# Optimization experiments

Hardware: AMD Instinct MI355X
Metric: run time of the kernel (lower is better)

## Reference

```python
import jax, jax.numpy as jnp
import numpy as np

B, S, D = 2, 2048, 1024          # batch, seq, hidden_dim
H, HD = 16, 64                   # heads, head_dim
R = 256                          # kv_lora_rank (MLA latent)
E, K, MH = 8, 2, 256             # n_experts, top_k, expert hidden
EPS = 1e-6
THETA = 10000.0


def setup_inputs() -> dict:
    key = jax.random.key(0)
    ks = jax.random.split(key, 11)
    init = lambda k, shape: jax.random.normal(k, shape, jnp.float32) * 0.02
    return {
        "x": jax.random.normal(ks[0], (B, S, D), jnp.float32),
        "position_ids": jnp.broadcast_to(jnp.arange(S, dtype=jnp.int32), (B, S)),
        "norm1_w": jnp.ones((D,), jnp.float32),
        "wq": init(ks[1], (D, H * HD)),
        "wdkv": init(ks[2], (D, R)),
        "wuk": init(ks[3], (R, H * HD)),
        "wuv": init(ks[4], (R, H * HD)),
        "wo": init(ks[5], (H * HD, D)),
        "norm2_w": jnp.ones((D,), jnp.float32),
        "wr": init(ks[6], (D, E)),
        "router_bias": jnp.zeros((E,), jnp.float32),
        "w1": init(ks[7], (E, D, MH)),
        "w3": init(ks[8], (E, D, MH)),
        "w2": init(ks[9], (E, MH, D)),
    }


def rmsnorm(x, w):
    var = jnp.mean(x * x, axis=-1, keepdims=True)
    return x * jax.lax.rsqrt(var + EPS) * w


def rope(q, k, pos):
    # q, k: [B,S,H,HD]; pos: [B,S]
    half = HD // 2
    inv = 1.0 / (THETA ** (jnp.arange(half, dtype=jnp.float32) / half))
    ang = pos[..., None].astype(jnp.float32) * inv        # [B,S,half]
    cos = jnp.cos(ang)[:, :, None, :]                     # [B,S,1,half]
    sin = jnp.sin(ang)[:, :, None, :]
    def rot(t):
        t1, t2 = t[..., :half], t[..., half:]
        return jnp.concatenate([t1 * cos - t2 * sin, t1 * sin + t2 * cos], -1)
    return rot(q), rot(k)


def mla_attention(x, pos, wq, wdkv, wuk, wuv, wo):
    q = (x @ wq).reshape(B, S, H, HD)
    c = x @ wdkv                                          # [B,S,R] latent KV
    k = (c @ wuk).reshape(B, S, H, HD)
    v = (c @ wuv).reshape(B, S, H, HD)
    q, k = rope(q, k, pos)
    scores = jnp.einsum('bqhd,bkhd->bhqk', q, k) / np.float32(np.sqrt(HD))
    causal = jnp.tril(jnp.ones((S, S), bool))
    scores = jnp.where(causal, scores, jnp.float32(-1e30))
    probs = jax.nn.softmax(scores, axis=-1)
    out = jnp.einsum('bhqk,bkhd->bqhd', probs, v).reshape(B, S, H * HD)
    return out @ wo


def self_adaptive_moe(x, wr, router_bias, w1, w3, w2):
    xf = x.reshape(-1, D)                                 # [T,D]
    scores = jax.nn.sigmoid(xf @ wr)                      # [T,E]
    # aux-loss-free balancing: bias only affects selection, not gate weights
    _, idx = jax.lax.top_k(scores + router_bias, K)       # [T,K]
    sel = jnp.take_along_axis(scores, idx, axis=1)        # [T,K]
    sel = sel / (jnp.sum(sel, -1, keepdims=True) + 1e-9)
    rows = jnp.arange(xf.shape[0])[:, None]
    gates = jnp.zeros_like(scores).at[rows, idx].set(sel)  # [T,E]
    y = jnp.zeros_like(xf)
    for e in range(E):  # small fixed expert count
        h = jax.nn.silu(xf @ w1[e]) * (xf @ w3[e])        # SwiGLU
        y = y + gates[:, e:e + 1] * (h @ w2[e])
    return y.reshape(B, S, D)


def reference(x, position_ids, norm1_w, wq, wdkv, wuk, wuv, wo,
              norm2_w, wr, router_bias, w1, w3, w2):
    x = x + mla_attention(rmsnorm(x, norm1_w), position_ids, wq, wdkv, wuk, wuv, wo)
    x = x + self_adaptive_moe(rmsnorm(x, norm2_w), wr, router_bias, w1, w3, w2)
    return x
```

## Files before the change

### kernel.cpp

```cpp
#include <hip/hip_runtime.h>
#include <hip/hip_bf16.h>
#include <math.h>


typedef __attribute__((ext_vector_type(8))) short short8;
typedef __attribute__((ext_vector_type(4))) float f32x4;

static __device__ __forceinline__ float bf2f(short s) {
  union { unsigned u; float f; } c; c.u = ((unsigned)(unsigned short)s) << 16; return c.f;
}
static __device__ __forceinline__ short f2bf(float f) {
  __hip_bfloat16 h = __float2bfloat16(f);
  short s; __builtin_memcpy(&s, &h, sizeof(s)); return s;
}
static __device__ __forceinline__ void split2(float v, short& hi, short& lo) {
  hi = f2bf(v); lo = f2bf(v - bf2f(hi));
}

__global__ void invtab_kernel(float* __restrict__ tab) {
  int j = threadIdx.x;
  if (j < 32) {
    float t = (float)pow(10000.0, (double)j * (1.0 / 32.0));
    tab[j] = 1.0f / t;
  }
}

__global__ __launch_bounds__(256) void rmsnorm_kernel(
    const float* __restrict__ in, const float* __restrict__ w,
    short* __restrict__ outH, short* __restrict__ outL,
    float* __restrict__ invrms)
{
  int row = blockIdx.x, tid = threadIdx.x;
  const float4* xv = (const float4*)(in + (size_t)row * 1024);
  float4 v = xv[tid];
  float ss = v.x*v.x + v.y*v.y + v.z*v.z + v.w*v.w;
  #pragma unroll
  for (int off = 32; off > 0; off >>= 1) ss += __shfl_down(ss, off);
  __shared__ float wsum[4];
  if ((tid & 63) == 0) wsum[tid >> 6] = ss;
  __syncthreads();
  float inv = rsqrtf((wsum[0] + wsum[1] + wsum[2] + wsum[3]) * (1.0f/1024.0f) + 1e-6f);
  float4 wv = ((const float4*)w)[tid];
  size_t base = (size_t)row * 1024 + (size_t)tid * 4;
  float r[4] = { v.x*inv*wv.x, v.y*inv*wv.y, v.z*inv*wv.z, v.w*inv*wv.w };
  #pragma unroll
  for (int j = 0; j < 4; ++j) {
    short hi, lo; split2(r[j], hi, lo);
    outH[base + j] = hi;
    if (outL) outL[base + j] = lo;
  }
  if (invrms && tid == 0) invrms[row] = inv;
}

template<bool SPLIT>
__global__ __launch_bounds__(256) void transpose_conv_kernel(
    const float* __restrict__ in, short* __restrict__ outH, short* __restrict__ outL,
    int K, int N, long zso, long ldo)
{
  __shared__ float tile[32][33];
  const float* ip = in + (size_t)blockIdx.z * K * N;
  size_t ob = (size_t)blockIdx.z * zso;
  int bn = blockIdx.x * 32, bk = blockIdx.y * 32;
  int tx = threadIdx.x & 31, ty = threadIdx.x >> 5;
  #pragma unroll
  for (int i = 0; i < 32; i += 8)
    tile[ty + i][tx] = ip[(size_t)(bk + ty + i) * N + bn + tx];
  __syncthreads();
  #pragma unroll
  for (int i = 0; i < 32; i += 8) {
    float v = tile[tx][ty + i];
    size_t oi = ob + (size_t)(bn + ty + i) * ldo + bk + tx;
    short hi, lo; split2(v, hi, lo);
    outH[oi] = hi;
    if (SPLIT) outL[oi] = lo;
  }
}

template<int EPI>
__global__ __launch_bounds__(256) void gemm_split_kernel(
    const short* __restrict__ AH, const short* __restrict__ AL,
    const short* __restrict__ BH, const short* __restrict__ BL,
    short* __restrict__ CH, short* __restrict__ CL,
    float* __restrict__ Cf, const float* __restrict__ res,
    int M, int N, int K)
{
  __shared__ __align__(16) short AsH[128*32], AsL[128*32], BsH[128*32], BsL[128*32];
  int bm = blockIdx.x * 128, bn = blockIdx.y * 128;
  int tid = threadIdx.x;
  int wave = tid >> 6, lane = tid & 63;
  int g = lane >> 4, r16 = lane & 15;
  int wr = wave >> 1, wc = wave & 1;
  f32x4 acc[4][4];
  #pragma unroll
  for (int m = 0; m < 4; ++m)
    #pragma unroll
    for (int n = 0; n < 4; ++n) acc[m][n] = (f32x4){0.f,0.f,0.f,0.f};
  int flat0 = tid * 8;
  for (int k0 = 0; k0 < K; k0 += 32) {
    __syncthreads();
    #pragma unroll
    for (int it = 0; it < 2; ++it) {
      int flat = it * 2048 + flat0;
      int row = flat >> 5, col = flat & 31;
      size_t ga = (size_t)(bm + row) * K + k0 + col;
      size_t gb = (size_t)(bn + row) * K + k0 + col;
      int lo = it * 4096 + wave * 1024;
      __builtin_amdgcn_global_load_lds((__attribute__((address_space(1))) void*)(AH + ga),
                                       (__attribute__((address_space(3))) void*)((char*)AsH + lo), 16, 0, 0);
      __builtin_amdgcn_global_load_lds((__attribute__((address_space(1))) void*)(AL + ga),
                                       (__attribute__((address_space(3))) void*)((char*)AsL + lo), 16, 0, 0);
      __builtin_amdgcn_global_load_lds((__attribute__((address_space(1))) void*)(BH + gb),
                                       (__attribute__((address_space(3))) void*)((char*)BsH + lo), 16, 0, 0);
      __builtin_amdgcn_global_load_lds((__attribute__((address_space(1))) void*)(BL + gb),
                                       (__attribute__((address_space(3))) void*)((char*)BsL + lo), 16, 0, 0);
    }
    __syncthreads();
    short8 afh[4], afl[4], bfh[4], bfl[4];
    #pragma unroll
    for (int m = 0; m < 4; ++m) {
      int off = (64*wr + 16*m + r16) * 32 + g * 8;
      afh[m] = *(const short8*)(AsH + off);
      afl[m] = *(const short8*)(AsL + off);
    }
    #pragma unroll
    for (int n = 0; n < 4; ++n) {
      int off = (64*wc + 16*n + r16) * 32 + g * 8;
      bfh[n] = *(const short8*)(BsH + off);
      bfl[n] = *(const short8*)(BsL + off);
    }
    #pragma unroll
    for (int m = 0; m < 4; ++m)
      #pragma unroll
      for (int n = 0; n < 4; ++n) {
        acc[m][n] = __builtin_amdgcn_mfma_f32_16x16x32_bf16(afh[m], bfh[n], acc[m][n], 0, 0, 0);
        acc[m][n] = __builtin_amdgcn_mfma_f32_16x16x32_bf16(afh[m], bfl[n], acc[m][n], 0, 0, 0);
        acc[m][n] = __builtin_amdgcn_mfma_f32_16x16x32_bf16(afl[m], bfh[n], acc[m][n], 0, 0, 0);
      }
  }
  #pragma unroll
  for (int m = 0; m < 4; ++m)
    #pragma unroll
    for (int n = 0; n < 4; ++n)
      #pragma unroll
      for (int r = 0; r < 4; ++r) {
        int row = bm + 64*wr + 16*m + g*4 + r;
        int col = bn + 64*wc + 16*n + r16;
        size_t idx = (size_t)row * N + col;
        float v = acc[m][n][r];
        if (EPI == 0) {
          short hi, lo; split2(v, hi, lo);
          CH[idx] = hi; CL[idx] = lo;
        } else {
          Cf[idx] = v + res[idx];
        }
      }
}

template<int EPI>
__global__ __launch_bounds__(256) void gemm_bt_kernel(
    const short* __restrict__ A, const short* __restrict__ Bt, void* __restrict__ Cv,
    const float* __restrict__ res,
    int M, int N, int K, long sBt, long sC, long ldC)
{
  __shared__ __align__(16) short As[128*32];
  __shared__ __align__(16) short Bs[128*32];
  int z = blockIdx.z;
  const short* Ab = A;
  const short* Bb = Bt + (size_t)z * sBt;
  int bm = blockIdx.x * 128, bn = blockIdx.y * 128;
  int tid = threadIdx.x;
  int wave = tid >> 6, lane = tid & 63;
  int g = lane >> 4, r16 = lane & 15;
  int wr = wave >> 1, wc = wave & 1;
  f32x4 acc[4][4];
  #pragma unroll
  for (int m = 0; m < 4; ++m)
    #pragma unroll
    for (int n = 0; n < 4; ++n) acc[m][n] = (f32x4){0.f,0.f,0.f,0.f};
  int flat0 = tid * 8;
  for (int k0 = 0; k0 < K; k0 += 32) {
    __syncthreads();
    #pragma unroll
    for (int it = 0; it < 2; ++it) {
      int flat = it * 2048 + flat0;
      int row = flat >> 5, col = flat & 31;
      const short* ga = Ab + (size_t)(bm + row) * K + k0 + col;
      const short* gb = Bb + (size_t)(bn + row) * K + k0 + col;
      char* la = (char*)As + it * 4096 + wave * 1024;
      char* lb = (char*)Bs + it * 4096 + wave * 1024;
      __builtin_amdgcn_global_load_lds((__attribute__((address_space(1))) void*)ga,
                                       (__attribute__((address_space(3))) void*)la, 16, 0, 0);
      __builtin_amdgcn_global_load_lds((__attribute__((address_space(1))) void*)gb,
                                       (__attribute__((address_space(3))) void*)lb, 16, 0, 0);
    }
    __syncthreads();
    short8 af[4], bfv[4];
    #pragma unroll
    for (int m = 0; m < 4; ++m)
      af[m] = *(const short8*)(As + (64*wr + 16*m + r16) * 32 + g * 8);
    #pragma unroll
    for (int n = 0; n < 4; ++n)
      bfv[n] = *(const short8*)(Bs + (64*wc + 16*n + r16) * 32 + g * 8);
    #pragma unroll
    for (int m = 0; m < 4; ++m)
      #pragma unroll
      for (int n = 0; n < 4; ++n)
        acc[m][n] = __builtin_amdgcn_mfma_f32_16x16x32_bf16(af[m], bfv[n], acc[m][n], 0, 0, 0);
  }
  #pragma unroll
  for (int m = 0; m < 4; ++m)
    #pragma unroll
    for (int n = 0; n < 4; ++n)
      #pragma unroll
      for (int r = 0; r < 4; ++r) {
        int row = bm + 64*wr + 16*m + g*4 + r;
        int col = bn + 64*wc + 16*n + r16;
        float v = acc[m][n][r];
        if (EPI == 0) {
          ((short*)Cv)[(size_t)z * sC + (size_t)row * ldC + col] = f2bf(v);
        } else {
          size_t idx = (size_t)row * N + col;
          ((float*)Cv)[idx] = v + res[idx];
        }
      }
}

__global__ __launch_bounds__(256) void rope_inplace_kernel(
    short* __restrict__ QH, short* __restrict__ QL,
    short* __restrict__ KH, short* __restrict__ KL,
    const int* __restrict__ pos_ids, const float* __restrict__ invtab)
{
  int token = blockIdx.x, tid = threadIdx.x;
  float pos = (float)pos_ids[token];
  #pragma unroll
  for (int it = 0; it < 2; ++it) {
    int p = it * 256 + tid;
    int h = p >> 5, j = p & 31;
    float ang = pos * invtab[j];
    float sn, cs; sincosf(ang, &sn, &cs);
    size_t i1 = (size_t)token * 1024 + h * 64 + j;
    size_t i2 = i1 + 32;
    float q1 = bf2f(QH[i1]) + bf2f(QL[i1]);
    float q2 = bf2f(QH[i2]) + bf2f(QL[i2]);
    float a = q1 * cs - q2 * sn, bq = q1 * sn + q2 * cs;
    short hi, lo;
    split2(a,  hi, lo); QH[i1] = hi; QL[i1] = lo;
    split2(bq, hi, lo); QH[i2] = hi; QL[i2] = lo;
    float k1 = bf2f(KH[i1]) + bf2f(KL[i1]);
    float k2 = bf2f(KH[i2]) + bf2f(KL[i2]);
    a = k1 * cs - k2 * sn; bq = k1 * sn + k2 * cs;
    split2(a,  hi, lo); KH[i1] = hi; KL[i1] = lo;
    split2(bq, hi, lo); KH[i2] = hi; KL[i2] = lo;
  }
}

__global__ __launch_bounds__(256) void v_tr_kernel(
    const short* __restrict__ VH, const short* __restrict__ VL,
    short* __restrict__ TH, short* __restrict__ TL)
{
  __shared__ short th[64][80], tl[64][80];
  int s0 = blockIdx.x * 64, bh = blockIdx.y;
  int b = bh >> 4, h = bh & 15;
  int tid = threadIdx.x;
  #pragma unroll
  for (int p = 0; p < 2; ++p) {
    int flat = p * 256 + tid;
    int sr = flat >> 3, ck = flat & 7;
    size_t gi = ((size_t)((b * 2048) + s0 + sr) * 16 + h) * 64 + ck * 8;
    short8 vh = *(const short8*)(VH + gi);
    short8 vl = *(const short8*)(VL + gi);
    #pragma unroll
    for (int i = 0; i < 8; ++i) { th[sr][ck*8+i] = vh[i]; tl[sr][ck*8+i] = vl[i]; }
  }
  __syncthreads();
  #pragma unroll
  for (int p = 0; p < 2; ++p) {
    int flat = p * 256 + tid;
    int dr = flat >> 3, sc = flat & 7;
    short8 rh, rl;
    #pragma unroll
    for (int i = 0; i < 8; ++i) { rh[i] = th[sc*8+i][dr]; rl[i] = tl[sc*8+i][dr]; }
    size_t go = ((size_t)bh * 64 + dr) * 2048 + s0 + sc * 8;
    *(short8*)(TH + go) = rh;
    *(short8*)(TL + go) = rl;
  }
}

__global__ __launch_bounds__(256) void attn_kernel(
    const short* __restrict__ QH, const short* __restrict__ QL,
    const short* __restrict__ KH, const short* __restrict__ KL,
    const short* __restrict__ VTH, const short* __restrict__ VTL,
    short* __restrict__ OH, short* __restrict__ OL)
{
  __shared__ __align__(16) char ksH[8192], ksL[8192], vtH[8192], vtL[8192];
  int qt = gridDim.x - 1 - blockIdx.x;
  int qb = qt * 64;
  int bh = blockIdx.y;
  int b = bh >> 4, h = bh & 15;
  int tid = threadIdx.x;
  int w = tid >> 6, lane = tid & 63;
  int g = lane >> 4, r16 = lane & 15;
  auto gidx = [&](int s, int d) -> size_t {
    return ((size_t)(b * 2048 + s) * 16 + h) * 64 + d;
  };
  int qrow = qb + 16 * w + r16;
  short8 qf0h = *(const short8*)(QH + gidx(qrow, g * 8));
  short8 qf0l = *(const short8*)(QL + gidx(qrow, g * 8));
  short8 qf1h = *(const short8*)(QH + gidx(qrow, 32 + g * 8));
  short8 qf1l = *(const short8*)(QL + gidx(qrow, 32 + g * 8));
  f32x4 o[4];
  #pragma unroll
  for (int c = 0; c < 4; ++c) o[c] = (f32x4){0.f,0.f,0.f,0.f};
  float mrun = -1e30f, lsum = 0.f;
  int qi = qrow;
  int nt = qt + 1;
  for (int t = 0; t < nt; ++t) {
    int kvb = t * 64;
    __syncthreads();
    #pragma unroll
    for (int i = 0; i < 2; ++i) {
      int wi = w * 2 + i;
      int row = wi * 8 + (lane >> 3);
      int cs = (lane & 7) ^ (row & 7);
      size_t gk = gidx(kvb + row, cs * 8);
      size_t gv = ((size_t)bh * 64 + row) * 2048 + kvb + cs * 8;
      int lb = wi * 1024;
      __builtin_amdgcn_global_load_lds((__attribute__((address_space(1))) void*)(KH + gk),
                                       (__attribute__((address_space(3))) void*)(ksH + lb), 16, 0, 0);
      __builtin_amdgcn_global_load_lds((__attribute__((address_space(1))) void*)(KL + gk),
                                       (__attribute__((address_space(3))) void*)(ksL + lb), 16, 0, 0);
      __builtin_amdgcn_global_load_lds((__attribute__((address_space(1))) void*)(VTH + gv),
                                       (__attribute__((address_space(3))) void*)(vtH + lb), 16, 0, 0);
      __builtin_amdgcn_global_load_lds((__attribute__((address_space(1))) void*)(VTL + gv),
                                       (__attribute__((address_space(3))) void*)(vtL + lb), 16, 0, 0);
    }
    __syncthreads();
    float p16[16]; float tm = -1e30f;
    #pragma unroll
    for (int T = 0; T < 4; ++T) {
      int krow = 16 * T + r16;
      int swz = (r16 & 7) << 4;
      short8 k0h = *(const short8*)(ksH + krow * 128 + ((16 * g) ^ swz));
      short8 k0l = *(const short8*)(ksL + krow * 128 + ((16 * g) ^ swz));
      short8 k1h = *(const short8*)(ksH + krow * 128 + ((64 + 16 * g) ^ swz));
      short8 k1l = *(const short8*)(ksL + krow * 128 + ((64 + 16 * g) ^ swz));
      f32x4 a = (f32x4){0.f,0.f,0.f,0.f};
      a = __builtin_amdgcn_mfma_f32_16x16x32_bf16(k0h, qf0h, a, 0, 0, 0);
      a = __builtin_amdgcn_mfma_f32_16x16x32_bf16(k0h, qf0l, a, 0, 0, 0);
      a = __builtin_amdgcn_mfma_f32_16x16x32_bf16(k0l, qf0h, a, 0, 0, 0);
      a = __builtin_amdgcn_mfma_f32_16x16x32_bf16(k1h, qf1h, a, 0, 0, 0);
      a = __builtin_amdgcn_mfma_f32_16x16x32_bf16(k1h, qf1l, a, 0, 0, 0);
      a = __builtin_amdgcn_mfma_f32_16x16x32_bf16(k1l, qf1h, a, 0, 0, 0);
      #pragma unroll
      for (int r = 0; r < 4; ++r) {
        float sv = a[r] * 0.125f;
        int kvi = kvb + 16 * T + 4 * g + r;
        sv = (kvi > qi) ? -1e30f : sv;
        p16[T * 4 + r] = sv;
        tm = fmaxf(tm, sv);
      }
    }
    tm = fmaxf(tm, __shfl_xor(tm, 16));
    tm = fmaxf(tm, __shfl_xor(tm, 32));
    float mnew = fmaxf(mrun, tm);
    float sf = __expf(mrun - mnew);
    float ps = 0.f;
    #pragma unroll
    for (int i2 = 0; i2 < 16; ++i2) { p16[i2] = __expf(p16[i2] - mnew); ps += p16[i2]; }
    ps += __shfl_xor(ps, 16);
    ps += __shfl_xor(ps, 32);
    lsum = lsum * sf + ps;
    mrun = mnew;
    float sfr[4];
    #pragma unroll
    for (int r = 0; r < 4; ++r) sfr[r] = __shfl(sf, 4 * g + r);
    #pragma unroll
    for (int c = 0; c < 4; ++c)
      #pragma unroll
      for (int r = 0; r < 4; ++r) o[c][r] *= sfr[r];
    short8 pah[2], pal[2];
    #pragma unroll
    for (int h2 = 0; h2 < 2; ++h2) {
      #pragma unroll
      for (int j = 0; j < 8; ++j) {
        int src = (((2 * g + (j >> 2)) & 3) << 4) + r16;
        float v0 = __shfl(p16[(2 * h2) * 4 + (j & 3)], src);
        float v1 = __shfl(p16[(2 * h2 + 1) * 4 + (j & 3)], src);
        float pv = (g >= 2) ? v1 : v0;
        short phi, plo; split2(pv, phi, plo);
        pah[h2][j] = phi; pal[h2][j] = plo;
      }
    }
    #pragma unroll
    for (int c = 0; c < 4; ++c) {
      #pragma unroll
      for (int h2 = 0; h2 < 2; ++h2) {
        int bo = (16 * c + r16) * 128 + ((64 * h2 + 16 * g) ^ ((r16 & 7) << 4));
        short8 vbh = *(const short8*)(vtH + bo);
        short8 vbl = *(const short8*)(vtL + bo);
        o[c] = __builtin_amdgcn_mfma_f32_16x16x32_bf16(pah[h2], vbh, o[c], 0, 0, 0);
        o[c] = __builtin_amdgcn_mfma_f32_16x16x32_bf16(pah[h2], vbl, o[c], 0, 0, 0);
        o[c] = __builtin_amdgcn_mfma_f32_16x16x32_bf16(pal[h2], vbh, o[c], 0, 0, 0);
      }
    }
  }
  float lr[4];
  #pragma unroll
  for (int r = 0; r < 4; ++r) lr[r] = __shfl(lsum, 4 * g + r);
  #pragma unroll
  for (int c = 0; c < 4; ++c)
    #pragma unroll
    for (int r = 0; r < 4; ++r) {
      int q = qb + 16 * w + 4 * g + r;
      int d = 16 * c + r16;
      float v = o[c][r] / lr[r];
      short hi, lo; split2(v, hi, lo);
      size_t oi = gidx(q, d);
      OH[oi] = hi; OL[oi] = lo;
    }
}

__global__ __launch_bounds__(256) void router_kernel(
    const float* __restrict__ xmid, const float* __restrict__ invrms,
    const float* __restrict__ w2norm, const float* __restrict__ wr,
    const float* __restrict__ rbias, float* __restrict__ gates)
{
  int row = blockIdx.x, tid = threadIdx.x;
  float invr = invrms[row];
  float part[8] = {0,0,0,0,0,0,0,0};
  for (int d = tid; d < 1024; d += 256) {
    float xv = xmid[(size_t)row * 1024 + d] * invr * w2norm[d];
    #pragma unroll
    for (int e = 0; e < 8; ++e) part[e] += xv * wr[d * 8 + e];
  }
  #pragma unroll
  for (int e = 0; e < 8; ++e)
    #pragma unroll
    for (int off = 32; off > 0; off >>= 1) part[e] += __shfl_down(part[e], off);
  __shared__ float red[4][8];
  if ((tid & 63) == 0)
    #pragma unroll
    for (int e = 0; e < 8; ++e) red[tid >> 6][e] = part[e];
  __syncthreads();
  if (tid == 0) {
    float sc[8], bs[8];
    #pragma unroll
    for (int e = 0; e < 8; ++e) {
      float t = red[0][e] + red[1][e] + red[2][e] + red[3][e];
      sc[e] = 1.f / (1.f + expf(-t));
      bs[e] = sc[e] + rbias[e];
    }
    int i0 = 0;
    #pragma unroll
    for (int e = 1; e < 8; ++e) if (bs[e] > bs[i0]) i0 = e;
    int i1 = -1;
    #pragma unroll
    for (int e = 0; e < 8; ++e) if (e != i0 && (i1 < 0 || bs[e] > bs[i1])) i1 = e;
    float s0 = sc[i0], s1 = sc[i1];
    float den = s0 + s1 + 1e-9f;
    #pragma unroll
    for (int e = 0; e < 8; ++e)
      gates[(size_t)row * 8 + e] = (e == i0) ? s0 / den : ((e == i1) ? s1 / den : 0.f);
  }
}

__global__ __launch_bounds__(256) void silu_gate_kernel(
    const short* __restrict__ h1, const short* __restrict__ h3,
    const float* __restrict__ gates, short* __restrict__ h)
{
  size_t i = ((size_t)blockIdx.x * 256 + threadIdx.x) * 8;
  int t = (int)(i >> 11);
  int e = (int)((i >> 8) & 7);
  float gv = gates[(size_t)t * 8 + e];
  short8 a = *(const short8*)(h1 + i);
  short8 b3 = *(const short8*)(h3 + i);
  short8 r;
  #pragma unroll
  for (int j = 0; j < 8; ++j) {
    float x = bf2f(a[j]);
    float y = bf2f(b3[j]);
    r[j] = f2bf(gv * (x / (1.f + expf(-x))) * y);
  }
  *(short8*)(h + i) = r;
}

#define MB (1048576ull)
enum : unsigned long long {
  OFF_WQTH  = 0*MB,  OFF_WQTL  = 2*MB,
  OFF_WDKVH = 4*MB,  OFF_WDKVL = 4*MB + 512*1024,
  OFF_WUKH  = 5*MB,  OFF_WUKL  = 5*MB + 512*1024,
  OFF_WUVH  = 6*MB,  OFF_WUVL  = 6*MB + 512*1024,
  OFF_WOTH  = 7*MB,  OFF_WOTL  = 9*MB,
  OFF_W1T   = 11*MB, OFF_W3T   = 15*MB, OFF_W2S = 19*MB,
  OFF_X1H   = 23*MB, OFF_X1L   = 31*MB,
  OFF_QTH   = 39*MB, OFF_QTL   = 47*MB,
  OFF_CH    = 55*MB, OFF_CL    = 57*MB,
  OFF_KTH   = 59*MB, OFF_KTL   = 67*MB,
  OFF_VTOKH = 75*MB, OFF_VTOKL = 83*MB,
  OFF_VT_H  = 23*MB, OFF_VT_L  = 31*MB,
  OFF_AOH   = 75*MB, OFF_AOL   = 83*MB,
  OFF_XMID  = 39*MB,
  OFF_X2    = 55*MB,
  OFF_H1    = 23*MB,
  OFF_H3    = 75*MB,
  OFF_INVT  = 91*MB,
  OFF_INVR  = 91*MB + 4096,
  OFF_GATES = 91*MB + 32768,
  WS_NEEDED = 91*MB + 262144
};

extern "C" void kernel_launch(void* const* d_in, const int* in_sizes, int n_in,
                              void* d_out, int out_size, void* d_ws, size_t ws_size,
                              hipStream_t stream) {
  const float* x     = (const float*)d_in[0];
  const int*   pos   = (const int*)d_in[1];
  const float* n1w   = (const float*)d_in[2];
  const float* wq    = (const float*)d_in[3];
  const float* wdkv  = (const float*)d_in[4];
  const float* wuk   = (const float*)d_in[5];
  const float* wuv   = (const float*)d_in[6];
  const float* wo    = (const float*)d_in[7];
  const float* n2w   = (const float*)d_in[8];
  const float* wr    = (const float*)d_in[9];
  const float* rbias = (const float*)d_in[10];
  const float* w1    = (const float*)d_in[11];
  const float* w3    = (const float*)d_in[12];
  const float* w2    = (const float*)d_in[13];
  float* out = (float*)d_out;
  char* ws = (char*)d_ws;
  if (ws_size < WS_NEEDED) return;

  short *WQTH=(short*)(ws+OFF_WQTH), *WQTL=(short*)(ws+OFF_WQTL);
  short *WDKVH=(short*)(ws+OFF_WDKVH), *WDKVL=(short*)(ws+OFF_WDKVL);
  short *WUKH=(short*)(ws+OFF_WUKH), *WUKL=(short*)(ws+OFF_WUKL);
  short *WUVH=(short*)(ws+OFF_WUVH), *WUVL=(short*)(ws+OFF_WUVL);
  short *WOTH=(short*)(ws+OFF_WOTH), *WOTL=(short*)(ws+OFF_WOTL);
  short *W1T=(short*)(ws+OFF_W1T), *W3T=(short*)(ws+OFF_W3T), *W2S=(short*)(ws+OFF_W2S);
  short *X1H=(short*)(ws+OFF_X1H), *X1L=(short*)(ws+OFF_X1L);
  short *QTH=(short*)(ws+OFF_QTH), *QTL=(short*)(ws+OFF_QTL);
  short *CH=(short*)(ws+OFF_CH),   *CL=(short*)(ws+OFF_CL);
  short *KTH=(short*)(ws+OFF_KTH), *KTL=(short*)(ws+OFF_KTL);
  short *VTOKH=(short*)(ws+OFF_VTOKH), *VTOKL=(short*)(ws+OFF_VTOKL);
  short *VT_H=(short*)(ws+OFF_VT_H), *VT_L=(short*)(ws+OFF_VT_L);
  short *AOH=(short*)(ws+OFF_AOH), *AOL=(short*)(ws+OFF_AOL);
  float *XMID=(float*)(ws+OFF_XMID);
  short *X2=(short*)(ws+OFF_X2);
  short *H1=(short*)(ws+OFF_H1), *H3=(short*)(ws+OFF_H3);
  float *INVT=(float*)(ws+OFF_INVT), *INVR=(float*)(ws+OFF_INVR), *GATES=(float*)(ws+OFF_GATES);

  invtab_kernel<<<1, 64, 0, stream>>>(INVT);
  rmsnorm_kernel<<<4096, 256, 0, stream>>>(x, n1w, X1H, X1L, nullptr);
  transpose_conv_kernel<true ><<<dim3(32,32,1), 256, 0, stream>>>(wq,   WQTH, WQTL, 1024, 1024, 0, 1024);
  transpose_conv_kernel<true ><<<dim3( 8,32,1), 256, 0, stream>>>(wdkv, WDKVH, WDKVL, 1024, 256, 0, 1024);
  transpose_conv_kernel<true ><<<dim3(32, 8,1), 256, 0, stream>>>(wuk,  WUKH, WUKL, 256, 1024, 0, 256);
  transpose_conv_kernel<true ><<<dim3(32, 8,1), 256, 0, stream>>>(wuv,  WUVH, WUVL, 256, 1024, 0, 256);
  transpose_conv_kernel<true ><<<dim3(32,32,1), 256, 0, stream>>>(wo,   WOTH, WOTL, 1024, 1024, 0, 1024);
  transpose_conv_kernel<false><<<dim3( 8,32,8), 256, 0, stream>>>(w1,   W1T, nullptr, 1024, 256, 262144, 1024);
  transpose_conv_kernel<false><<<dim3( 8,32,8), 256, 0, stream>>>(w3,   W3T, nullptr, 1024, 256, 262144, 1024);
  transpose_conv_kernel<false><<<dim3(32, 8,8), 256, 0, stream>>>(w2,   W2S, nullptr, 256, 1024, 256, 2048);
  gemm_split_kernel<0><<<dim3(32,8), 256, 0, stream>>>(X1H, X1L, WQTH, WQTL, QTH, QTL, nullptr, nullptr, 4096, 1024, 1024);
  gemm_split_kernel<0><<<dim3(32,2), 256, 0, stream>>>(X1H, X1L, WDKVH, WDKVL, CH, CL, nullptr, nullptr, 4096, 256, 1024);
  gemm_split_kernel<0><<<dim3(32,8), 256, 0, stream>>>(CH, CL, WUKH, WUKL, KTH, KTL, nullptr, nullptr, 4096, 1024, 256);
  gemm_split_kernel<0><<<dim3(32,8), 256, 0, stream>>>(CH, CL, WUVH, WUVL, VTOKH, VTOKL, nullptr, nullptr, 4096, 1024, 256);
  v_tr_kernel<<<dim3(32,32), 256, 0, stream>>>(VTOKH, VTOKL, VT_H, VT_L);
  rope_inplace_kernel<<<4096, 256, 0, stream>>>(QTH, QTL, KTH, KTL, pos, INVT);
  attn_kernel<<<dim3(32,32), 256, 0, stream>>>(QTH, QTL, KTH, KTL, VT_H, VT_L, AOH, AOL);
  gemm_split_kernel<1><<<dim3(32,8), 256, 0, stream>>>(AOH, AOL, WOTH, WOTL, nullptr, nullptr, XMID, x, 4096, 1024, 1024);
  rmsnorm_kernel<<<4096, 256, 0, stream>>>(XMID, n2w, X2, nullptr, INVR);
  router_kernel<<<4096, 256, 0, stream>>>(XMID, INVR, n2w, wr, rbias, GATES);
  gemm_bt_kernel<0><<<dim3(32,2,8), 256, 0, stream>>>(X2, W1T, H1, nullptr, 4096, 256, 1024, 262144, 256, 2048);
  gemm_bt_kernel<0><<<dim3(32,2,8), 256, 0, stream>>>(X2, W3T, H3, nullptr, 4096, 256, 1024, 262144, 256, 2048);
  silu_gate_kernel<<<4096, 256, 0, stream>>>(H1, H3, GATES, H1);
  gemm_bt_kernel<1><<<dim3(32,8,1), 256, 0, stream>>>(H1, W2S, out, XMID, 4096, 1024, 2048, 0, 0, 0);
}
```

Baseline: 604.3 us.

## Fuse router into rmsnorm, SwiGLU gating into GEMM epilogue, double-buffer attention

The second RMSNorm now also computes router logits, sigmoid, top-2 selection and gate weights in the same kernel, which removes a separate router pass over XMID. The SiLU-and-gate step moves into the epilogue of the W3 expert GEMM, which removes the standalone elementwise kernel and a round trip of H1/H3 through memory. The attention kernel double-buffers its K/V shared-memory tiles so the next tile loads while the current one computes, and each block handles a pair of query tiles (qt and 31-qt) to even out the causal workload across half as many blocks. Shared memory per attention block doubles, which may reduce occupancy.

```diff
diff --git a/kernel.cpp b/kernel.cpp
--- a/kernel.cpp
+++ b/kernel.cpp
@@ -16,6 +16,9 @@
 static __device__ __forceinline__ void split2(float v, short& hi, short& lo) {
   hi = f2bf(v); lo = f2bf(v - bf2f(hi));
 }
+#define GLD16(gp, lp) __builtin_amdgcn_global_load_lds( \
+    (__attribute__((address_space(1))) void*)(gp), \
+    (__attribute__((address_space(3))) void*)(lp), 16, 0, 0)
 
 __global__ void invtab_kernel(float* __restrict__ tab) {
   int j = threadIdx.x;
@@ -27,8 +30,7 @@
 
 __global__ __launch_bounds__(256) void rmsnorm_kernel(
     const float* __restrict__ in, const float* __restrict__ w,
-    short* __restrict__ outH, short* __restrict__ outL,
-    float* __restrict__ invrms)
+    short* __restrict__ outH, short* __restrict__ outL)
 {
   int row = blockIdx.x, tid = threadIdx.x;
   const float4* xv = (const float4*)(in + (size_t)row * 1024);
@@ -49,7 +51,63 @@
     outH[base + j] = hi;
     if (outL) outL[base + j] = lo;
   }
-  if (invrms && tid == 0) invrms[row] = inv;
+}
+
+__global__ __launch_bounds__(256) void rmsnorm_router_kernel(
+    const float* __restrict__ in, const float* __restrict__ w,
+    short* __restrict__ outH,
+    const float* __restrict__ wr, const float* __restrict__ rbias,
+    float* __restrict__ gates)
+{
+  int row = blockIdx.x, tid = threadIdx.x;
+  float4 v = ((const float4*)(in + (size_t)row * 1024))[tid];
+  float ss = v.x*v.x + v.y*v.y + v.z*v.z + v.w*v.w;
+  #pragma unroll
+  for (int off = 32; off > 0; off >>= 1) ss += __shfl_down(ss, off);
+  __shared__ float wsum[4];
+  if ((tid & 63) == 0) wsum[tid >> 6] = ss;
+  __syncthreads();
+  float inv = rsqrtf((wsum[0] + wsum[1] + wsum[2] + wsum[3]) * (1.0f/1024.0f) + 1e-6f);
+  float4 wv = ((const float4*)w)[tid];
+  size_t base = (size_t)row * 1024 + (size_t)tid * 4;
+  float r[4] = { v.x*inv*wv.x, v.y*inv*wv.y, v.z*inv*wv.z, v.w*inv*wv.w };
+  #pragma unroll
+  for (int j = 0; j < 4; ++j) outH[base + j] = f2bf(r[j]);
+  float part[8] = {0,0,0,0,0,0,0,0};
+  const float* wrp = wr + (size_t)tid * 32;
+  #pragma unroll
+  for (int j = 0; j < 4; ++j)
+    #pragma unroll
+    for (int e = 0; e < 8; ++e) part[e] += r[j] * wrp[j * 8 + e];
+  #pragma unroll
+  for (int e = 0; e < 8; ++e)
+    #pragma unroll
+    for (int off = 32; off > 0; off >>= 1) part[e] += __shfl_down(part[e], off);
+  __shared__ float red[4][8];
+  if ((tid & 63) == 0)
+    #pragma unroll
+    for (int e = 0; e < 8; ++e) red[tid >> 6][e] = part[e];
+  __syncthreads();
+  if (tid == 0) {
+    float sc[8], bs[8];
+    #pragma unroll
+    for (int e = 0; e < 8; ++e) {
+      float t = red[0][e] + red[1][e] + red[2][e] + red[3][e];
+      sc[e] = 1.f / (1.f + expf(-t));
+      bs[e] = sc[e] + rbias[e];
+    }
+    int i0 = 0;
+    #pragma unroll
+    for (int e = 1; e < 8; ++e) if (bs[e] > bs[i0]) i0 = e;
+    int i1 = -1;
+    #pragma unroll
+    for (int e = 0; e < 8; ++e) if (e != i0 && (i1 < 0 || bs[e] > bs[i1])) i1 = e;
+    float s0 = sc[i0], s1 = sc[i1];
+    float den = s0 + s1 + 1e-9f;
+    #pragma unroll
+    for (int e = 0; e < 8; ++e)
+      gates[(size_t)row * 8 + e] = (e == i0) ? s0 / den : ((e == i1) ? s1 / den : 0.f);
+  }
 }
 
 template<bool SPLIT>
@@ -105,14 +163,10 @@
       size_t ga = (size_t)(bm + row) * K + k0 + col;
       size_t gb = (size_t)(bn + row) * K + k0 + col;
       int lo = it * 4096 + wave * 1024;
-      __builtin_amdgcn_global_load_lds((__attribute__((address_space(1))) void*)(AH + ga),
-                                       (__attribute__((address_space(3))) void*)((char*)AsH + lo), 16, 0, 0);
-      __builtin_amdgcn_global_load_lds((__attribute__((address_space(1))) void*)(AL + ga),
-                                       (__attribute__((address_space(3))) void*)((char*)AsL + lo), 16, 0, 0);
-      __builtin_amdgcn_global_load_lds((__attribute__((address_space(1))) void*)(BH + gb),
-                                       (__attribute__((address_space(3))) void*)((char*)BsH + lo), 16, 0, 0);
-      __builtin_amdgcn_global_load_lds((__attribute__((address_space(1))) void*)(BL + gb),
-                                       (__attribute__((address_space(3))) void*)((char*)BsL + lo), 16, 0, 0);
+      GLD16(AH + ga, (char*)AsH + lo);
+      GLD16(AL + ga, (char*)AsL + lo);
+      GLD16(BH + gb, (char*)BsH + lo);
+      GLD16(BL + gb, (char*)BsL + lo);
     }
     __syncthreads();
     short8 afh[4], afl[4], bfh[4], bfl[4];
@@ -159,7 +213,8 @@
 template<int EPI>
 __global__ __launch_bounds__(256) void gemm_bt_kernel(
     const short* __restrict__ A, const short* __restrict__ Bt, void* __restrict__ Cv,
-    const float* __restrict__ res,
+    const float* __restrict__ res, const short* __restrict__ aux,
+    const float* __restrict__ gates,
     int M, int N, int K, long sBt, long sC, long ldC)
 {
   __shared__ __align__(16) short As[128*32];
@@ -184,14 +239,8 @@
     for (int it = 0; it < 2; ++it) {
       int flat = it * 2048 + flat0;
       int row = flat >> 5, col = flat & 31;
-      const short* ga = Ab + (size_t)(bm + row) * K + k0 + col;
-      const short* gb = Bb + (size_t)(bn + row) * K + k0 + col;
-      char* la = (char*)As + it * 4096 + wave * 1024;
-      char* lb = (char*)Bs + it * 4096 + wave * 1024;
-      __builtin_amdgcn_global_load_lds((__attribute__((address_space(1))) void*)ga,
-                                       (__attribute__((address_space(3))) void*)la, 16, 0, 0);
-      __builtin_amdgcn_global_load_lds((__attribute__((address_space(1))) void*)gb,
-                                       (__attribute__((address_space(3))) void*)lb, 16, 0, 0);
+      GLD16(Ab + (size_t)(bm + row) * K + k0 + col, (char*)As + it * 4096 + wave * 1024);
+      GLD16(Bb + (size_t)(bn + row) * K + k0 + col, (char*)Bs + it * 4096 + wave * 1024);
     }
     __syncthreads();
     short8 af[4], bfv[4];
@@ -218,9 +267,14 @@
         float v = acc[m][n][r];
         if (EPI == 0) {
           ((short*)Cv)[(size_t)z * sC + (size_t)row * ldC + col] = f2bf(v);
-        } else {
+        } else if (EPI == 1) {
           size_t idx = (size_t)row * N + col;
           ((float*)Cv)[idx] = v + res[idx];
+        } else {
+          size_t oi = (size_t)z * sC + (size_t)row * ldC + col;
+          float xv = bf2f(aux[oi]);
+          float gv = gates[(size_t)row * 8 + z];
+          ((short*)Cv)[oi] = f2bf(gv * (xv / (1.f + expf(-xv))) * v);
         }
       }
 }
@@ -292,9 +346,8 @@
     const short* __restrict__ VTH, const short* __restrict__ VTL,
     short* __restrict__ OH, short* __restrict__ OL)
 {
-  __shared__ __align__(16) char ksH[8192], ksL[8192], vtH[8192], vtL[8192];
-  int qt = gridDim.x - 1 - blockIdx.x;
-  int qb = qt * 64;
+  __shared__ __align__(16) char ksH[2][8192], ksL[2][8192], vtH[2][8192], vtL[2][8192];
+  int bx = blockIdx.x;
   int bh = blockIdx.y;
   int b = bh >> 4, h = bh & 15;
   int tid = threadIdx.x;
@@ -303,185 +356,128 @@
   auto gidx = [&](int s, int d) -> size_t {
     return ((size_t)(b * 2048 + s) * 16 + h) * 64 + d;
   };
-  int qrow = qb + 16 * w + r16;
-  short8 qf0h = *(const short8*)(QH + gidx(qrow, g * 8));
-  short8 qf0l = *(const short8*)(QL + gidx(qrow, g * 8));
-  short8 qf1h = *(const short8*)(QH + gidx(qrow, 32 + g * 8));
-  short8 qf1l = *(const short8*)(QL + gidx(qrow, 32 + g * 8));
-  f32x4 o[4];
-  #pragma unroll
-  for (int c = 0; c < 4; ++c) o[c] = (f32x4){0.f,0.f,0.f,0.f};
-  float mrun = -1e30f, lsum = 0.f;
-  int qi = qrow;
-  int nt = qt + 1;
-  for (int t = 0; t < nt; ++t) {
+  int srow = lane >> 3, cs0 = lane & 7;
+  auto stage = [&](int t, int buf) {
     int kvb = t * 64;
-    __syncthreads();
     #pragma unroll
     for (int i = 0; i < 2; ++i) {
       int wi = w * 2 + i;
-      int row = wi * 8 + (lane >> 3);
-      int cs = (lane & 7) ^ (row & 7);
+      int row = wi * 8 + srow;
+      int cs = cs0 ^ (row & 7);
       size_t gk = gidx(kvb + row, cs * 8);
       size_t gv = ((size_t)bh * 64 + row) * 2048 + kvb + cs * 8;
       int lb = wi * 1024;
-      __builtin_amdgcn_global_load_lds((__attribute__((address_space(1))) void*)(KH + gk),
-                                       (__attribute__((address_space(3))) void*)(ksH + lb), 16, 0, 0);
-      __builtin_amdgcn_global_load_lds((__attribute__((address_space(1))) void*)(KL + gk),
-                                       (__attribute__((address_space(3))) void*)(ksL + lb), 16, 0, 0);
-      __builtin_amdgcn_global_load_lds((__attribute__((address_space(1))) void*)(VTH + gv),
-                                       (__attribute__((address_space(3))) void*)(vtH + lb), 16, 0, 0);
-      __builtin_amdgcn_global_load_lds((__attribute__((address_space(1))) void*)(VTL + gv),
-                                       (__attribute__((address_space(3))) void*)(vtL + lb), 16, 0, 0);
-    }
-    __syncthreads();
-    float p16[16]; float tm = -1e30f;
-    #pragma unroll
-    for (int T = 0; T < 4; ++T) {
-      int krow = 16 * T + r16;
-      int swz = (r16 & 7) << 4;
-      short8 k0h = *(const short8*)(ksH + krow * 128 + ((16 * g) ^ swz));
-      short8 k0l = *(const short8*)(ksL + krow * 128 + ((16 * g) ^ swz));
-      short8 k1h = *(const short8*)(ksH + krow * 128 + ((64 + 16 * g) ^ swz));
-      short8 k1l = *(const short8*)(ksL + krow * 128 + ((64 + 16 * g) ^ swz));
-      f32x4 a = (f32x4){0.f,0.f,0.f,0.f};
-      a = __builtin_amdgcn_mfma_f32_16x16x32_bf16(k0h, qf0h, a, 0, 0, 0);
-      a = __builtin_amdgcn_mfma_f32_16x16x32_bf16(k0h, qf0l, a, 0, 0, 0);
-      a = __builtin_amdgcn_mfma_f32_16x16x32_bf16(k0l, qf0h, a, 0, 0, 0);
-      a = __builtin_amdgcn_mfma_f32_16x16x32_bf16(k1h, qf1h, a, 0, 0, 0);
-      a = __builtin_amdgcn_mfma_f32_16x16x32_bf16(k1h, qf1l, a, 0, 0, 0);
-      a = __builtin_amdgcn_mfma_f32_16x16x32_bf16(k1l, qf1h, a, 0, 0, 0);
+      GLD16(KH + gk,  &ksH[buf][lb]);
+      GLD16(KL + gk,  &ksL[buf][lb]);
+      GLD16(VTH + gv, &vtH[buf][lb]);
+      GLD16(VTL + gv, &vtL[buf][lb]);
+    }
+  };
+  for (int half = 0; half < 2; ++half) {
+    int qt = half ? bx : (31 - bx);
+    int qb = qt * 64;
+    int qrow = qb + 16 * w + r16;
+    short8 qf0h = *(const short8*)(QH + gidx(qrow, g * 8));
+    short8 qf0l = *(const short8*)(QL + gidx(qrow, g * 8));
+    short8 qf1h = *(const short8*)(QH + gidx(qrow, 32 + g * 8));
+    short8 qf1l = *(const short8*)(QL + gidx(qrow, 32 + g * 8));
+    f32x4 o[4];
+    #pragma unroll
+    for (int c = 0; c < 4; ++c) o[c] = (f32x4){0.f,0.f,0.f,0.f};
+    float mrun = -1e30f, lsum = 0.f;
+    int qi = qrow;
+    int nt = qt + 1;
+    int cur = 0;
+    stage(0, cur);
+    for (int t = 0; t < nt; ++t) {
+      __syncthreads();
+      if (t + 1 < nt) stage(t + 1, cur ^ 1);
+      int kvb = t * 64;
+      float p16[16]; float tm = -1e30f;
+      #pragma unroll
+      for (int T = 0; T < 4; ++T) {
+        int krow = 16 * T + r16;
+        int swz = (r16 & 7) << 4;
+        short8 k0h = *(const short8*)(&ksH[cur][krow * 128 + ((16 * g) ^ swz)]);
+        short8 k0l = *(const short8*)(&ksL[cur][krow * 128 + ((16 * g) ^ swz)]);
+        short8 k1h = *(const short8*)(&ksH[cur][krow * 128 + ((64 + 16 * g) ^ swz)]);
+        short8 k1l = *(const short8*)(&ksL[cur][krow * 128 + ((64 + 16 * g) ^ swz)]);
+        f32x4 a = (f32x4){0.f,0.f,0.f,0.f};
+        a = __builtin_amdgcn_mfma_f32_16x16x32_bf16(k0h, qf0h, a, 0, 0, 0);
+        a = __builtin_amdgcn_mfma_f32_16x16x32_bf16(k0h, qf0l, a, 0, 0, 0);
+        a = __builtin_amdgcn_mfma_f32_16x16x32_bf16(k0l, qf0h, a, 0, 0, 0);
+        a = __builtin_amdgcn_mfma_f32_16x16x32_bf16(k1h, qf1h, a, 0, 0, 0);
+        a = __builtin_amdgcn_mfma_f32_16x16x32_bf16(k1h, qf1l, a, 0, 0, 0);
+        a = __builtin_amdgcn_mfma_f32_16x16x32_bf16(k1l, qf1h, a, 0, 0, 0);
+        #pragma unroll
+        for (int r = 0; r < 4; ++r) {
+          float sv = a[r] * 0.125f;
+          int kvi = kvb + 16 * T + 4 * g + r;
+          sv = (kvi > qi) ? -1e30f : sv;
+          p16[T * 4 + r] = sv;
+          tm = fmaxf(tm, sv);
+        }
+      }
+      tm = fmaxf(tm, __shfl_xor(tm, 16));
+      tm = fmaxf(tm, __shfl_xor(tm, 32));
+      float mnew = fmaxf(mrun, tm);
+      float sf = __expf(mrun - mnew);
+      float ps = 0.f;
+      #pragma unroll
+      for (int i2 = 0; i2 < 16; ++i2) { p16[i2] = __expf(p16[i2] - mnew); ps += p16[i2]; }
+      ps += __shfl_xor(ps, 16);
+      ps += __shfl_xor(ps, 32);
+      lsum = lsum * sf + ps;
+      mrun = mnew;
+      float sfr[4];
+      #pragma unroll
+      for (int r = 0; r < 4; ++r) sfr[r] = __shfl(sf, 4 * g + r);
+      #pragma unroll
+      for (int c = 0; c < 4; ++c)
+        #pragma unroll
+        for (int r = 0; r < 4; ++r) o[c][r] *= sfr[r];
+      short8 pah[2], pal[2];
+      #pragma unroll
+      for (int h2 = 0; h2 < 2; ++h2) {
+        #pragma unroll
+        for (int j = 0; j < 8; ++j) {
+          int src = (((2 * g + (j >> 2)) & 3) << 4) + r16;
+          float v0 = __shfl(p16[(2 * h2) * 4 + (j & 3)], src);
+          float v1 = __shfl(p16[(2 * h2 + 1) * 4 + (j & 3)], src);
+          float pv = (g >= 2) ? v1 : v0;
+          short phi, plo; split2(pv, phi, plo);
+          pah[h2][j] = phi; pal[h2][j] = plo;
+        }
+      }
+      #pragma unroll
+      for (int c = 0; c < 4; ++c) {
+        #pragma unroll
+        for (int h2 = 0; h2 < 2; ++h2) {
+          int bo = (16 * c + r16) * 128 + ((64 * h2 + 16 * g) ^ ((r16 & 7) << 4));
+          short8 vbh = *(const short8*)(&vtH[cur][bo]);
+          short8 vbl = *(const short8*)(&vtL[cur][bo]);
+          o[c] = __builtin_amdgcn_mfma_f32_16x16x32_bf16(pah[h2], vbh, o[c], 0, 0, 0);
+          o[c] = __builtin_amdgcn_mfma_f32_16x16x32_bf16(pah[h2], vbl, o[c], 0, 0, 0);
+          o[c] = __builtin_amdgcn_mfma_f32_16x16x32_bf16(pal[h2], vbh, o[c], 0, 0, 0);
+        }
+      }
+      cur ^= 1;
+    }
+    float lr[4];
+    #pragma unroll
+    for (int r = 0; r < 4; ++r) lr[r] = __shfl(lsum, 4 * g + r);
+    #pragma unroll
+    for (int c = 0; c < 4; ++c)
       #pragma unroll
       for (int r = 0; r < 4; ++r) {
-        float sv = a[r] * 0.125f;
-        int kvi = kvb + 16 * T + 4 * g + r;
-        sv = (kvi > qi) ? -1e30f : sv;
-        p16[T * 4 + r] = sv;
-        tm = fmaxf(tm, sv);
-      }
-    }
-    tm = fmaxf(tm, __shfl_xor(tm, 16));
-    tm = fmaxf(tm, __shfl_xor(tm, 32));
-    float mnew = fmaxf(mrun, tm);
-    float sf = __expf(mrun - mnew);
-    float ps = 0.f;
-    #pragma unroll
-    for (int i2 = 0; i2 < 16; ++i2) { p16[i2] = __expf(p16[i2] - mnew); ps += p16[i2]; }
-    ps += __shfl_xor(ps, 16);
-    ps += __shfl_xor(ps, 32);
-    lsum = lsum * sf + ps;
-    mrun = mnew;
-    float sfr[4];
-    #pragma unroll
-    for (int r = 0; r < 4; ++r) sfr[r] = __shfl(sf, 4 * g + r);
-    #pragma unroll
-    for (int c = 0; c < 4; ++c)
-      #pragma unroll
-      for (int r = 0; r < 4; ++r) o[c][r] *= sfr[r];
-    short8 pah[2], pal[2];
-    #pragma unroll
-    for (int h2 = 0; h2 < 2; ++h2) {
-      #pragma unroll
-      for (int j = 0; j < 8; ++j) {
-        int src = (((2 * g + (j >> 2)) & 3) << 4) + r16;
-        float v0 = __shfl(p16[(2 * h2) * 4 + (j & 3)], src);
-        float v1 = __shfl(p16[(2 * h2 + 1) * 4 + (j & 3)], src);
-        float pv = (g >= 2) ? v1 : v0;
-        short phi, plo; split2(pv, phi, plo);
-        pah[h2][j] = phi; pal[h2][j] = plo;
-      }
-    }
-    #pragma unroll
-    for (int c = 0; c < 4; ++c) {
-      #pragma unroll
-      for (int h2 = 0; h2 < 2; ++h2) {
-        int bo = (16 * c + r16) * 128 + ((64 * h2 + 16 * g) ^ ((r16 & 7) << 4));
-        short8 vbh = *(const short8*)(vtH + bo);
-        short8 vbl = *(const short8*)(vtL + bo);
-        o[c] = __builtin_amdgcn_mfma_f32_16x16x32_bf16(pah[h2], vbh, o[c], 0, 0, 0);
-        o[c] = __builtin_amdgcn_mfma_f32_16x16x32_bf16(pah[h2], vbl, o[c], 0, 0, 0);
-        o[c] = __builtin_amdgcn_mfma_f32_16x16x32_bf16(pal[h2], vbh, o[c], 0, 0, 0);
-      }
-    }
-  }
-  float lr[4];
-  #pragma unroll
-  for (int r = 0; r < 4; ++r) lr[r] = __shfl(lsum, 4 * g + r);
-  #pragma unroll
-  for (int c = 0; c < 4; ++c)
-    #pragma unroll
-    for (int r = 0; r < 4; ++r) {
-      int q = qb + 16 * w + 4 * g + r;
-      int d = 16 * c + r16;
-      float v = o[c][r] / lr[r];
-      short hi, lo; split2(v, hi, lo);
-      size_t oi = gidx(q, d);
-      OH[oi] = hi; OL[oi] = lo;
-    }
-}
-
-__global__ __launch_bounds__(256) void router_kernel(
-    const float* __restrict__ xmid, const float* __restrict__ invrms,
-    const float* __restrict__ w2norm, const float* __restrict__ wr,
-    const float* __restrict__ rbias, float* __restrict__ gates)
-{
-  int row = blockIdx.x, tid = threadIdx.x;
-  float invr = invrms[row];
-  float part[8] = {0,0,0,0,0,0,0,0};
-  for (int d = tid; d < 1024; d += 256) {
-    float xv = xmid[(size_t)row * 1024 + d] * invr * w2norm[d];
-    #pragma unroll
-    for (int e = 0; e < 8; ++e) part[e] += xv * wr[d * 8 + e];
-  }
-  #pragma unroll
-  for (int e = 0; e < 8; ++e)
-    #pragma unroll
-    for (int off = 32; off > 0; off >>= 1) part[e] += __shfl_down(part[e], off);
-  __shared__ float red[4][8];
-  if ((tid & 63) == 0)
-    #pragma unroll
-    for (int e = 0; e < 8; ++e) red[tid >> 6][e] = part[e];
-  __syncthreads();
-  if (tid == 0) {
-    float sc[8], bs[8];
-    #pragma unroll
-    for (int e = 0; e < 8; ++e) {
-      float t = red[0][e] + red[1][e] + red[2][e] + red[3][e];
-      sc[e] = 1.f / (1.f + expf(-t));
-      bs[e] = sc[e] + rbias[e];
-    }
-    int i0 = 0;
-    #pragma unroll
-    for (int e = 1; e < 8; ++e) if (bs[e] > bs[i0]) i0 = e;
-    int i1 = -1;
-    #pragma unroll
-    for (int e = 0; e < 8; ++e) if (e != i0 && (i1 < 0 || bs[e] > bs[i1])) i1 = e;
-    float s0 = sc[i0], s1 = sc[i1];
-    float den = s0 + s1 + 1e-9f;
-    #pragma unroll
-    for (int e = 0; e < 8; ++e)
-      gates[(size_t)row * 8 + e] = (e == i0) ? s0 / den : ((e == i1) ? s1 / den : 0.f);
-  }
-}
-
-__global__ __launch_bounds__(256) void silu_gate_kernel(
-    const short* __restrict__ h1, const short* __restrict__ h3,
-    const float* __restrict__ gates, short* __restrict__ h)
-{
-  size_t i = ((size_t)blockIdx.x * 256 + threadIdx.x) * 8;
-  int t = (int)(i >> 11);
-  int e = (int)((i >> 8) & 7);
-  float gv = gates[(size_t)t * 8 + e];
-  short8 a = *(const short8*)(h1 + i);
-  short8 b3 = *(const short8*)(h3 + i);
-  short8 r;
-  #pragma unroll
-  for (int j = 0; j < 8; ++j) {
-    float x = bf2f(a[j]);
-    float y = bf2f(b3[j]);
-    r[j] = f2bf(gv * (x / (1.f + expf(-x))) * y);
-  }
-  *(short8*)(h + i) = r;
+        int q = qb + 16 * w + 4 * g + r;
+        int d = 16 * c + r16;
+        float v = o[c][r] / lr[r];
+        short hi, lo; split2(v, hi, lo);
+        size_t oi = gidx(q, d);
+        OH[oi] = hi; OL[oi] = lo;
+      }
+  }
 }
 
 #define MB (1048576ull)
@@ -504,7 +500,6 @@
   OFF_H1    = 23*MB,
   OFF_H3    = 75*MB,
   OFF_INVT  = 91*MB,
-  OFF_INVR  = 91*MB + 4096,
   OFF_GATES = 91*MB + 32768,
   WS_NEEDED = 91*MB + 262144
 };
@@ -546,10 +541,10 @@
   float *XMID=(float*)(ws+OFF_XMID);
   short *X2=(short*)(ws+OFF_X2);
   short *H1=(short*)(ws+OFF_H1), *H3=(short*)(ws+OFF_H3);
-  float *INVT=(float*)(ws+OFF_INVT), *INVR=(float*)(ws+OFF_INVR), *GATES=(float*)(ws+OFF_GATES);
+  float *INVT=(float*)(ws+OFF_INVT), *GATES=(float*)(ws+OFF_GATES);
 
   invtab_kernel<<<1, 64, 0, stream>>>(INVT);
-  rmsnorm_kernel<<<4096, 256, 0, stream>>>(x, n1w, X1H, X1L, nullptr);
+  rmsnorm_kernel<<<4096, 256, 0, stream>>>(x, n1w, X1H, X1L);
   transpose_conv_kernel<true ><<<dim3(32,32,1), 256, 0, stream>>>(wq,   WQTH, WQTL, 1024, 1024, 0, 1024);
   transpose_conv_kernel<true ><<<dim3( 8,32,1), 256, 0, stream>>>(wdkv, WDKVH, WDKVL, 1024, 256, 0, 1024);
   transpose_conv_kernel<true ><<<dim3(32, 8,1), 256, 0, stream>>>(wuk,  WUKH, WUKL, 256, 1024, 0, 256);
@@ -564,12 +559,10 @@
   gemm_split_kernel<0><<<dim3(32,8), 256, 0, stream>>>(CH, CL, WUVH, WUVL, VTOKH, VTOKL, nullptr, nullptr, 4096, 1024, 256);
   v_tr_kernel<<<dim3(32,32), 256, 0, stream>>>(VTOKH, VTOKL, VT_H, VT_L);
   rope_inplace_kernel<<<4096, 256, 0, stream>>>(QTH, QTL, KTH, KTL, pos, INVT);
-  attn_kernel<<<dim3(32,32), 256, 0, stream>>>(QTH, QTL, KTH, KTL, VT_H, VT_L, AOH, AOL);
+  attn_kernel<<<dim3(16,32), 256, 0, stream>>>(QTH, QTL, KTH, KTL, VT_H, VT_L, AOH, AOL);
   gemm_split_kernel<1><<<dim3(32,8), 256, 0, stream>>>(AOH, AOL, WOTH, WOTL, nullptr, nullptr, XMID, x, 4096, 1024, 1024);
-  rmsnorm_kernel<<<4096, 256, 0, stream>>>(XMID, n2w, X2, nullptr, INVR);
-  router_kernel<<<4096, 256, 0, stream>>>(XMID, INVR, n2w, wr, rbias, GATES);
-  gemm_bt_kernel<0><<<dim3(32,2,8), 256, 0, stream>>>(X2, W1T, H1, nullptr, 4096, 256, 1024, 262144, 256, 2048);
-  gemm_bt_kernel<0><<<dim3(32,2,8), 256, 0, stream>>>(X2, W3T, H3, nullptr, 4096, 256, 1024, 262144, 256, 2048);
-  silu_gate_kernel<<<4096, 256, 0, stream>>>(H1, H3, GATES, H1);
-  gemm_bt_kernel<1><<<dim3(32,8,1), 256, 0, stream>>>(H1, W2S, out, XMID, 4096, 1024, 2048, 0, 0, 0);
-}
+  rmsnorm_router_kernel<<<4096, 256, 0, stream>>>(XMID, n2w, X2, wr, rbias, GATES);
+  gemm_bt_kernel<0><<<dim3(32,2,8), 256, 0, stream>>>(X2, W1T, H1, nullptr, nullptr, nullptr, 4096, 256, 1024, 262144, 256, 2048);
+  gemm_bt_kernel<2><<<dim3(32,2,8), 256, 0, stream>>>(X2, W3T, H3, nullptr, H1, GATES, 4096, 256, 1024, 262144, 256, 2048);
+  gemm_bt_kernel<1><<<dim3(32,8,1), 256, 0, stream>>>(H3, W2S, out, XMID, nullptr, nullptr, 4096, 1024, 2048, 0, 0, 0);
+}
```

Measured after the change: 548.3 us. 9.3% less time.
